# Kernel tuning notes

Measured on AMD Instinct MI355X. Metric: run time of the kernel, lower is better.

The kernel has to match this reference:

```python
import jax, jax.numpy as jnp
import numpy as np

RADIUS = 1.0  # from init_kwargs
B = 8388608

def setup_inputs() -> dict:
    key = jax.random.key(0)
    k1, k2 = jax.random.split(key)
    x = jax.random.normal(k1, (B, 3), dtype=jnp.float32)
    center = jax.random.normal(k2, (B, 3), dtype=jnp.float32)
    return {"x": x, "center": center}

def reference(x, center):
    # Closed-form solution of: min ||z - x||^2  s.t. ||z - center||^2 <= r^2
    # z = x if inside the ball, else center + r * (x - center)/||x - center||
    d = x - center                                   # [B, 3]
    n = jnp.linalg.norm(d, axis=-1, keepdims=True)   # [B, 1]
    scale = jnp.minimum(jnp.float32(1.0), RADIUS / jnp.maximum(n, jnp.float32(1e-12)))
    return center + d * scale
```

## Files before the change

### kernel.cpp

```cpp
#include <hip/hip_runtime.h>


#define RADIUS 1.0f

__global__ __launch_bounds__(256) void circle_proj_lds(
    const float4* __restrict__ xv,
    const float4* __restrict__ cv,
    float4* __restrict__ ov)
{
    __shared__ float4 sx[768];
    __shared__ float4 sc[768];

    const int tid = threadIdx.x;
    const long base = (long)blockIdx.x * 768 + tid;

#pragma unroll
    for (int k = 0; k < 3; ++k) {
        sx[k*256 + tid] = xv[base + k*256];
        sc[k*256 + tid] = cv[base + k*256];
    }
    __syncthreads();

    float4 x0 = sx[3*tid + 0], x1 = sx[3*tid + 1], x2 = sx[3*tid + 2];
    float4 c0 = sc[3*tid + 0], c1 = sc[3*tid + 1], c2 = sc[3*tid + 2];

    float px[12] = {x0.x, x0.y, x0.z, x0.w, x1.x, x1.y, x1.z, x1.w, x2.x, x2.y, x2.z, x2.w};
    float pc[12] = {c0.x, c0.y, c0.z, c0.w, c1.x, c1.y, c1.z, c1.w, c2.x, c2.y, c2.z, c2.w};
    float po[12];

#pragma unroll
    for (int p = 0; p < 4; ++p) {
        float dx = px[3*p + 0] - pc[3*p + 0];
        float dy = px[3*p + 1] - pc[3*p + 1];
        float dz = px[3*p + 2] - pc[3*p + 2];
        float n2 = dx*dx + dy*dy + dz*dz;
        float n  = sqrtf(n2);
        float denom = fmaxf(n, 1e-12f);
        float scale = fminf(1.0f, RADIUS / denom);
        po[3*p + 0] = pc[3*p + 0] + dx * scale;
        po[3*p + 1] = pc[3*p + 1] + dy * scale;
        po[3*p + 2] = pc[3*p + 2] + dz * scale;
    }

    __syncthreads();
    sx[3*tid + 0] = make_float4(po[0], po[1], po[2],  po[3]);
    sx[3*tid + 1] = make_float4(po[4], po[5], po[6],  po[7]);
    sx[3*tid + 2] = make_float4(po[8], po[9], po[10], po[11]);
    __syncthreads();

#pragma unroll
    for (int k = 0; k < 3; ++k) {
        ov[base + k*256] = sx[k*256 + tid];
    }
}

__global__ __launch_bounds__(256) void circle_proj_tail(
    const float* __restrict__ x,
    const float* __restrict__ c,
    float* __restrict__ o,
    long start_pt, long npts)
{
    long p = start_pt + blockIdx.x * blockDim.x + threadIdx.x;
    if (p >= npts) return;
    float dx = x[3*p+0] - c[3*p+0];
    float dy = x[3*p+1] - c[3*p+1];
    float dz = x[3*p+2] - c[3*p+2];
    float n = sqrtf(dx*dx + dy*dy + dz*dz);
    float scale = fminf(1.0f, RADIUS / fmaxf(n, 1e-12f));
    o[3*p+0] = c[3*p+0] + dx * scale;
    o[3*p+1] = c[3*p+1] + dy * scale;
    o[3*p+2] = c[3*p+2] + dz * scale;
}

extern "C" void kernel_launch(void* const* d_in, const int* in_sizes, int n_in,
                              void* d_out, int out_size, void* d_ws, size_t ws_size,
                              hipStream_t stream) {
    const float* x = (const float*)d_in[0];
    const float* c = (const float*)d_in[1];
    float* out = (float*)d_out;

    long total_floats = in_sizes[0];
    long nf4 = total_floats / 4;
    long ntiles = nf4 / 768;

    if (ntiles > 0) {
        circle_proj_lds<<<(int)ntiles, 256, 0, stream>>>(
            (const float4*)x, (const float4*)c, (float4*)out);
    }

    long pts_done = ntiles * 1024;
    long npts = total_floats / 3;
    if (pts_done < npts) {
        long rem = npts - pts_done;
        int grid = (int)((rem + 255) / 256);
        circle_proj_tail<<<grid, 256, 0, stream>>>(x, c, out, pts_done, npts);
    }
}
```

Baseline: 241.7 us.

## Use persistent per-wave LDS transpose with register prefetch and nontemporal stores

Replaces the one-tile-per-block kernel with a persistent grid of at most 1024 blocks. Each wavefront owns its own LDS slice, which lets a waitcnt fence replace block-wide barriers. Each wave prefetches the next chunk into registers while it computes and stores the current one, and writes the output with nontemporal stores. The sqrt-plus-divide is replaced by rsqrt with a squared epsilon. The aim is better overlap of memory latency and less sync overhead, at the cost of a capped grid that may not fill the device's bandwidth and rsqrt's slightly different rounding.

```diff
diff --git a/kernel.cpp b/kernel.cpp
--- a/kernel.cpp
+++ b/kernel.cpp
@@ -3,54 +3,88 @@
 
 #define RADIUS 1.0f
 
-__global__ __launch_bounds__(256) void circle_proj_lds(
+typedef float f32x4 __attribute__((ext_vector_type(4)));
+
+#define WAVE_LDS_FENCE() asm volatile("s_waitcnt lgkmcnt(0)" ::: "memory")
+
+__global__ __launch_bounds__(256, 4) void circle_proj_wave(
     const float4* __restrict__ xv,
     const float4* __restrict__ cv,
-    float4* __restrict__ ov)
+    float4* __restrict__ ov,
+    long nchunks)
 {
-    __shared__ float4 sx[768];
-    __shared__ float4 sc[768];
+    __shared__ float4 sx[4][192];
+    __shared__ float4 sc[4][192];
 
-    const int tid = threadIdx.x;
-    const long base = (long)blockIdx.x * 768 + tid;
+    const int wid  = threadIdx.x >> 6;
+    const int lane = threadIdx.x & 63;
+    float4* wx = sx[wid];
+    float4* wc = sc[wid];
+
+    const long nw = (long)gridDim.x * 4;
+    long ch = (long)blockIdx.x * 4 + wid;
+    if (ch >= nchunks) return;
+
+    long b = ch * 192 + lane;
+    float4 r0 = xv[b], r1 = xv[b + 64], r2 = xv[b + 128];
+    float4 s0 = cv[b], s1 = cv[b + 64], s2 = cv[b + 128];
+
+    while (true) {
+        const long chn  = ch + nw;
+        const bool more = (chn < nchunks);
+
+        float4 t0, t1, t2, u0, u1, u2;
+        if (more) {
+            const long bn = chn * 192 + lane;
+            t0 = xv[bn]; t1 = xv[bn + 64]; t2 = xv[bn + 128];
+            u0 = cv[bn]; u1 = cv[bn + 64]; u2 = cv[bn + 128];
+        }
+
+        wx[lane] = r0; wx[lane + 64] = r1; wx[lane + 128] = r2;
+        wc[lane] = s0; wc[lane + 64] = s1; wc[lane + 128] = s2;
+
+        WAVE_LDS_FENCE();
+
+        const float4 x0 = wx[3*lane + 0], x1 = wx[3*lane + 1], x2 = wx[3*lane + 2];
+        const float4 c0 = wc[3*lane + 0], c1 = wc[3*lane + 1], c2 = wc[3*lane + 2];
+
+        const float px[12] = {x0.x, x0.y, x0.z, x0.w, x1.x, x1.y, x1.z, x1.w, x2.x, x2.y, x2.z, x2.w};
+        const float pc[12] = {c0.x, c0.y, c0.z, c0.w, c1.x, c1.y, c1.z, c1.w, c2.x, c2.y, c2.z, c2.w};
+        float po[12];
 
 #pragma unroll
-    for (int k = 0; k < 3; ++k) {
-        sx[k*256 + tid] = xv[base + k*256];
-        sc[k*256 + tid] = cv[base + k*256];
-    }
-    __syncthreads();
+        for (int p = 0; p < 4; ++p) {
+            const float dx = px[3*p + 0] - pc[3*p + 0];
+            const float dy = px[3*p + 1] - pc[3*p + 1];
+            const float dz = px[3*p + 2] - pc[3*p + 2];
+            const float n2 = dx*dx + dy*dy + dz*dz;
+            const float scale = fminf(1.0f, RADIUS * rsqrtf(fmaxf(n2, 1e-24f)));
+            po[3*p + 0] = pc[3*p + 0] + dx * scale;
+            po[3*p + 1] = pc[3*p + 1] + dy * scale;
+            po[3*p + 2] = pc[3*p + 2] + dz * scale;
+        }
 
-    float4 x0 = sx[3*tid + 0], x1 = sx[3*tid + 1], x2 = sx[3*tid + 2];
-    float4 c0 = sc[3*tid + 0], c1 = sc[3*tid + 1], c2 = sc[3*tid + 2];
+        wx[3*lane + 0] = make_float4(po[0], po[1], po[2],  po[3]);
+        wx[3*lane + 1] = make_float4(po[4], po[5], po[6],  po[7]);
+        wx[3*lane + 2] = make_float4(po[8], po[9], po[10], po[11]);
 
-    float px[12] = {x0.x, x0.y, x0.z, x0.w, x1.x, x1.y, x1.z, x1.w, x2.x, x2.y, x2.z, x2.w};
-    float pc[12] = {c0.x, c0.y, c0.z, c0.w, c1.x, c1.y, c1.z, c1.w, c2.x, c2.y, c2.z, c2.w};
-    float po[12];
+        WAVE_LDS_FENCE();
 
-#pragma unroll
-    for (int p = 0; p < 4; ++p) {
-        float dx = px[3*p + 0] - pc[3*p + 0];
-        float dy = px[3*p + 1] - pc[3*p + 1];
-        float dz = px[3*p + 2] - pc[3*p + 2];
-        float n2 = dx*dx + dy*dy + dz*dz;
-        float n  = sqrtf(n2);
-        float denom = fmaxf(n, 1e-12f);
-        float scale = fminf(1.0f, RADIUS / denom);
-        po[3*p + 0] = pc[3*p + 0] + dx * scale;
-        po[3*p + 1] = pc[3*p + 1] + dy * scale;
-        po[3*p + 2] = pc[3*p + 2] + dz * scale;
-    }
+        const float4 o0 = wx[lane], o1 = wx[lane + 64], o2 = wx[lane + 128];
+        const long ob = ch * 192 + lane;
+        {
+            const f32x4 v0 = {o0.x, o0.y, o0.z, o0.w};
+            const f32x4 v1 = {o1.x, o1.y, o1.z, o1.w};
+            const f32x4 v2 = {o2.x, o2.y, o2.z, o2.w};
+            __builtin_nontemporal_store(v0, (f32x4*)&ov[ob]);
+            __builtin_nontemporal_store(v1, (f32x4*)&ov[ob + 64]);
+            __builtin_nontemporal_store(v2, (f32x4*)&ov[ob + 128]);
+        }
 
-    __syncthreads();
-    sx[3*tid + 0] = make_float4(po[0], po[1], po[2],  po[3]);
-    sx[3*tid + 1] = make_float4(po[4], po[5], po[6],  po[7]);
-    sx[3*tid + 2] = make_float4(po[8], po[9], po[10], po[11]);
-    __syncthreads();
-
-#pragma unroll
-    for (int k = 0; k < 3; ++k) {
-        ov[base + k*256] = sx[k*256 + tid];
+        if (!more) break;
+        r0 = t0; r1 = t1; r2 = t2;
+        s0 = u0; s1 = u1; s2 = u2;
+        ch = chn;
     }
 }
 
@@ -81,14 +115,16 @@
 
     long total_floats = in_sizes[0];
     long nf4 = total_floats / 4;
-    long ntiles = nf4 / 768;
+    long nchunks = nf4 / 192;
 
-    if (ntiles > 0) {
-        circle_proj_lds<<<(int)ntiles, 256, 0, stream>>>(
-            (const float4*)x, (const float4*)c, (float4*)out);
+    if (nchunks > 0) {
+        long blocks = (nchunks + 3) / 4;
+        if (blocks > 1024) blocks = 1024;
+        circle_proj_wave<<<(int)blocks, 256, 0, stream>>>(
+            (const float4*)x, (const float4*)c, (float4*)out, nchunks);
     }
 
-    long pts_done = ntiles * 1024;
+    long pts_done = nchunks * 256;
     long npts = total_floats / 3;
     if (pts_done < npts) {
         long rem = npts - pts_done;
```

Result: slower. 247.3 us (+2.4%).

## Replace LDS transpose with wave-shuffle segmented norms in grid-stride streaming kernel

Applied to the files above, without the earlier changes.

The shared-memory tile transpose is removed. Each lane now loads one float4 directly, and the per-point squared norms that straddle float4 boundaries are combined across neighbouring lanes with shuffles, using a 63-lane chunk of 84 points per wave. The launch becomes a capped grid-stride loop with an occupancy hint, and the divide plus sqrt is replaced by rsqrt. This drops the LDS traffic and block barriers, at the cost of one idle lane per wave, an unaligned 63-float4 chunk stride, and slightly different rounding from rsqrt.

```diff
diff --git a/kernel.cpp b/kernel.cpp
--- a/kernel.cpp
+++ b/kernel.cpp
@@ -3,54 +3,54 @@
 
 #define RADIUS 1.0f
 
-__global__ __launch_bounds__(256) void circle_proj_lds(
+__global__ __launch_bounds__(256, 8) void circle_proj_stream(
     const float4* __restrict__ xv,
     const float4* __restrict__ cv,
-    float4* __restrict__ ov)
+    float4* __restrict__ ov,
+    long nchunks)
 {
-    __shared__ float4 sx[768];
-    __shared__ float4 sc[768];
+    const int wid   = threadIdx.x >> 6;
+    const int lane  = threadIdx.x & 63;
+    const int phase = lane % 3;
+    const bool ph0  = (phase == 0);
+    const bool ph2  = (phase == 2);
+    const bool b1   = (phase < 2);
 
-    const int tid = threadIdx.x;
-    const long base = (long)blockIdx.x * 768 + tid;
+    const long nw = (long)gridDim.x * 4;
+    const bool active = (lane < 63);
 
-#pragma unroll
-    for (int k = 0; k < 3; ++k) {
-        sx[k*256 + tid] = xv[base + k*256];
-        sc[k*256 + tid] = cv[base + k*256];
-    }
-    __syncthreads();
+    for (long ch = (long)blockIdx.x * 4 + wid; ch < nchunks; ch += nw) {
+        const long f = ch * 63 + lane;
 
-    float4 x0 = sx[3*tid + 0], x1 = sx[3*tid + 1], x2 = sx[3*tid + 2];
-    float4 c0 = sc[3*tid + 0], c1 = sc[3*tid + 1], c2 = sc[3*tid + 2];
+        float4 x4 = make_float4(0.f, 0.f, 0.f, 0.f);
+        float4 c4 = make_float4(0.f, 0.f, 0.f, 0.f);
+        if (active) { x4 = xv[f]; c4 = cv[f]; }
 
-    float px[12] = {x0.x, x0.y, x0.z, x0.w, x1.x, x1.y, x1.z, x1.w, x2.x, x2.y, x2.z, x2.w};
-    float pc[12] = {c0.x, c0.y, c0.z, c0.w, c1.x, c1.y, c1.z, c1.w, c2.x, c2.y, c2.z, c2.w};
-    float po[12];
+        const float d0 = x4.x - c4.x, d1 = x4.y - c4.y;
+        const float d2 = x4.z - c4.z, d3 = x4.w - c4.w;
+        const float q0 = d0*d0, q1 = d1*d1, q2 = d2*d2, q3 = d3*d3;
 
-#pragma unroll
-    for (int p = 0; p < 4; ++p) {
-        float dx = px[3*p + 0] - pc[3*p + 0];
-        float dy = px[3*p + 1] - pc[3*p + 1];
-        float dz = px[3*p + 2] - pc[3*p + 2];
-        float n2 = dx*dx + dy*dy + dz*dz;
-        float n  = sqrtf(n2);
-        float denom = fmaxf(n, 1e-12f);
-        float scale = fminf(1.0f, RADIUS / denom);
-        po[3*p + 0] = pc[3*p + 0] + dx * scale;
-        po[3*p + 1] = pc[3*p + 1] + dy * scale;
-        po[3*p + 2] = pc[3*p + 2] + dz * scale;
-    }
+        const float hp = q0 + (b1  ? q1 : 0.0f) + (ph0 ? q2 : 0.0f);
+        const float tp = q3 + (!ph0 ? q2 : 0.0f) + (ph2 ? q1 : 0.0f);
 
-    __syncthreads();
-    sx[3*tid + 0] = make_float4(po[0], po[1], po[2],  po[3]);
-    sx[3*tid + 1] = make_float4(po[4], po[5], po[6],  po[7]);
-    sx[3*tid + 2] = make_float4(po[8], po[9], po[10], po[11]);
-    __syncthreads();
+        const float hp_next = __shfl_down(hp, 1, 64);
+        const float tp_prev = __shfl_up(tp, 1, 64);
 
-#pragma unroll
-    for (int k = 0; k < 3; ++k) {
-        ov[base + k*256] = sx[k*256 + tid];
+        const float n2h = hp + (ph0 ? 0.0f : tp_prev);
+        const float n2t = tp + (ph2 ? 0.0f : hp_next);
+
+        const float sh = fminf(1.0f, RADIUS * rsqrtf(fmaxf(n2h, 1e-24f)));
+        const float st = fminf(1.0f, RADIUS * rsqrtf(fmaxf(n2t, 1e-24f)));
+
+        const float s0 = sh;
+        const float s1 = b1  ? sh : st;
+        const float s2 = ph0 ? sh : st;
+        const float s3 = st;
+
+        if (active) {
+            ov[f] = make_float4(c4.x + d0*s0, c4.y + d1*s1,
+                                c4.z + d2*s2, c4.w + d3*s3);
+        }
     }
 }
 
@@ -81,14 +81,16 @@
 
     long total_floats = in_sizes[0];
     long nf4 = total_floats / 4;
-    long ntiles = nf4 / 768;
+    long nchunks = nf4 / 63;
 
-    if (ntiles > 0) {
-        circle_proj_lds<<<(int)ntiles, 256, 0, stream>>>(
-            (const float4*)x, (const float4*)c, (float4*)out);
+    if (nchunks > 0) {
+        long blocks = (nchunks + 3) / 4;
+        if (blocks > 2048) blocks = 2048;
+        circle_proj_stream<<<(int)blocks, 256, 0, stream>>>(
+            (const float4*)x, (const float4*)c, (float4*)out, nchunks);
     }
 
-    long pts_done = ntiles * 1024;
+    long pts_done = nchunks * 84;
     long npts = total_floats / 3;
     if (pts_done < npts) {
         long rem = npts - pts_done;
```

Measured after the change: 246.9 us. 1.02x slower.
